# Kernel optimization log

Measured on AMD Instinct MI355X. Metric: run time of the kernel, lower is better.

The kernel has to match this reference:

```python
import jax, jax.numpy as jnp
import numpy as np

LN_EPS = 1e-5

def _ln(x):
    # haiku LayerNorm([-1], create_scale=False, create_offset=False)
    mu = x.mean(axis=-1, keepdims=True)
    var = x.var(axis=-1, keepdims=True)
    return (x - mu) * jax.lax.rsqrt(var + LN_EPS)

def setup_inputs() -> dict:
    key = jax.random.key(0)
    ks = jax.random.split(key, 10)
    N, L, P = 512, 256, 64
    inp = {
        "local": jax.random.normal(ks[0], (N, L), jnp.float32),
        "pair": jax.random.normal(ks[1], (N, N, P), jnp.float32),
        "mask": jax.random.randint(ks[2], (N,), 0, 2, jnp.int32),
        "W_pair_gate": jax.random.normal(ks[3], (P, 2 * P), jnp.float32) / np.sqrt(P),
        "W_pair_value": jax.random.normal(ks[4], (P, 2 * P), jnp.float32) / np.sqrt(P),
        "W_left_gate": jax.random.normal(ks[5], (L, 2 * P), jnp.float32) / np.sqrt(L),
        "W_left_value": jax.random.normal(ks[6], (L, 2 * P), jnp.float32) / np.sqrt(L),
        "W_right_gate": jax.random.normal(ks[7], (L, 2 * P), jnp.float32) / np.sqrt(L),
        "W_right_value": jax.random.normal(ks[8], (L, 2 * P), jnp.float32) / np.sqrt(L),
        "W_out": jax.random.normal(ks[9], (3 * P, P), jnp.float32) / np.sqrt(3 * P),
    }
    return inp

def reference(local, pair, mask, W_pair_gate, W_pair_value, W_left_gate,
              W_left_value, W_right_gate, W_right_value, W_out):
    maskb = mask.astype(bool)
    pair_mask = maskb[:, None] & maskb[None, :]                  # (N, N)
    l = _ln(local)                                               # (N, L)
    p = _ln(pair)                                                # (N, N, P)
    pair_gate = p @ W_pair_gate                                  # (N, N, 2P)
    pair_value = p @ W_pair_value                                # (N, N, 2P)
    # left: broadcast local over axis 0/1, gelu-gate, mask, reduce over j
    left_gate = jax.nn.gelu((l @ W_left_gate)[:, None] + pair_gate)
    left_value = (l @ W_left_value)[None, :] + pair_value
    left = jnp.where(pair_mask[..., None], left_gate * left_value, 0).sum(axis=1)  # (N, 2P)
    right_gate = jax.nn.gelu((l @ W_right_gate)[None, :] + pair_gate)
    right_value = (l @ W_right_value)[:, None] + pair_value
    right = jnp.where(pair_mask[..., None], right_gate * right_value, 0).sum(axis=0)  # (N, 2P)
    paired_pseudo_local = _ln(left[:, None] + right[None, :])    # (N, N, 2P)
    pair_hidden = jnp.concatenate((p, paired_pseudo_local), axis=-1)  # (N, N, 3P)
    return pair_hidden @ W_out                                   # (N, N, P)
```

## Files before the change

### kernel.cpp

```cpp
#include <hip/hip_runtime.h>
#include <math.h>

#define LN_EPS 1e-5f


typedef __bf16 bf16x8 __attribute__((ext_vector_type(8)));
typedef float f32x16 __attribute__((ext_vector_type(16)));

__device__ __forceinline__ float gelu_f(float x) {
    float x2 = x * x;
    float e = __builtin_amdgcn_exp2f(x * fmaf(0.10294423f, x2, 2.3022079f));
    float r = __builtin_amdgcn_rcpf(e + 1.0f);
    return fmaf(-x, r, x);
}

__global__ __launch_bounds__(256) void kA(
    const float* __restrict__ loc,
    const float* __restrict__ Wlg, const float* __restrict__ Wlv,
    const float* __restrict__ Wrg, const float* __restrict__ Wrv,
    float* __restrict__ proj, const int* __restrict__ mask,
    int* __restrict__ act, float* __restrict__ left, float* __restrict__ right) {
    const int t = threadIdx.x;
    if (blockIdx.x == 64) {
        if (blockIdx.y == 1) {
            float4 z = {0.f, 0.f, 0.f, 0.f};
            for (int idx = t; idx < 16384; idx += 256) ((float4*)left)[idx] = z;
        } else if (blockIdx.y == 2) {
            float4 z = {0.f, 0.f, 0.f, 0.f};
            for (int idx = t; idx < 16384; idx += 256) ((float4*)right)[idx] = z;
        } else if (blockIdx.y == 0) {
            __shared__ int cnt_sh[8];
            const int lane = t & 63, wv = t >> 6;
            int msave[2];
            unsigned long long bsave[2];
#pragma unroll
            for (int ch = 0; ch < 2; ++ch) {
                int m = (mask[ch * 256 + t] != 0);
                unsigned long long b = __ballot(m);
                if (lane == 0) cnt_sh[ch * 4 + wv] = __popcll(b);
                msave[ch] = m;
                bsave[ch] = b;
            }
            __syncthreads();
#pragma unroll
            for (int ch = 0; ch < 2; ++ch) {
                int base = 0;
                for (int u = 0; u < ch * 4 + wv; ++u) base += cnt_sh[u];
                int pos = base + __popcll(bsave[ch] & ((1ull << lane) - 1ull));
                if (msave[ch]) act[1 + pos] = ch * 256 + t;
            }
            if (t == 0) {
                int ctot = 0;
                for (int u = 0; u < 8; ++u) ctot += cnt_sh[u];
                act[0] = ctot;
            }
        }
        return;
    }
    __shared__ float ln_sh[8][260];
    __shared__ float red_sh[128][9];
    const int i0 = blockIdx.x * 8;
    const int mat = blockIdx.y;
    const float* __restrict__ W = (mat == 0) ? Wlg : (mat == 1) ? Wlv
                                 : (mat == 2) ? Wrg : Wrv;
    {
        int row = t >> 5, l32 = t & 31;
        const float4* src = (const float4*)(loc + (i0 + row) * 256);
        float4 v0 = src[l32 * 2];
        float4 v1 = src[l32 * 2 + 1];
        float s = (v0.x + v0.y) + (v0.z + v0.w) + (v1.x + v1.y) + (v1.z + v1.w);
        float ss = v0.x * v0.x + v0.y * v0.y + v0.z * v0.z + v0.w * v0.w +
                   v1.x * v1.x + v1.y * v1.y + v1.z * v1.z + v1.w * v1.w;
#pragma unroll
        for (int off = 1; off < 32; off <<= 1) {
            s += __shfl_xor(s, off);
            ss += __shfl_xor(ss, off);
        }
        float mu = s * (1.f / 256.f);
        float rs = rsqrtf(ss * (1.f / 256.f) - mu * mu + LN_EPS);
        float4 o0, o1;
        o0.x = (v0.x - mu) * rs; o0.y = (v0.y - mu) * rs;
        o0.z = (v0.z - mu) * rs; o0.w = (v0.w - mu) * rs;
        o1.x = (v1.x - mu) * rs; o1.y = (v1.y - mu) * rs;
        o1.z = (v1.z - mu) * rs; o1.w = (v1.w - mu) * rs;
        *(float4*)&ln_sh[row][l32 * 8] = o0;
        *(float4*)&ln_sh[row][l32 * 8 + 4] = o1;
    }
    __syncthreads();

    const int n = t & 127;
    const int kh = t >> 7;
    float acc[8] = {0.f, 0.f, 0.f, 0.f, 0.f, 0.f, 0.f, 0.f};
#pragma unroll 2
    for (int c = 0; c < 32; ++c) {
        const int kc = kh * 128 + c * 4;
        float w0 = W[(kc + 0) * 128 + n];
        float w1 = W[(kc + 1) * 128 + n];
        float w2 = W[(kc + 2) * 128 + n];
        float w3 = W[(kc + 3) * 128 + n];
#pragma unroll
        for (int r = 0; r < 8; ++r) {
            float4 l4 = *(const float4*)&ln_sh[r][kc];
            acc[r] += l4.x * w0 + l4.y * w1 + l4.z * w2 + l4.w * w3;
        }
    }
    if (kh == 1) {
#pragma unroll
        for (int r = 0; r < 8; ++r) red_sh[n][r] = acc[r];
    }
    __syncthreads();
    if (kh == 0) {
#pragma unroll
        for (int r = 0; r < 8; ++r)
            proj[mat * 65536 + (i0 + r) * 128 + n] = acc[r] + red_sh[n][r];
    }
}

#define KB_TI 8
__global__ __launch_bounds__(256) void kB(
    const float* __restrict__ pair, const int* __restrict__ act,
    const float* __restrict__ Wg, const float* __restrict__ Wv,
    const float* __restrict__ lg, const float* __restrict__ lv,
    const float* __restrict__ rg, const float* __restrict__ rv,
    float* __restrict__ left, float* __restrict__ right) {
    __shared__ __bf16 A_sh[2][32][72];
    __shared__ int ji_sh[32];
    __shared__ int ii_sh[KB_TI];

    const int cnt = act[0];
    const int j0 = blockIdx.x * 32;
    const int ibase = blockIdx.y * KB_TI;
    if (j0 >= cnt || ibase >= cnt) return;
    const int nact = min(KB_TI, cnt - ibase);

    const int t = threadIdx.x;
    const int lane = t & 63;
    const int w = t >> 6;
    const int c = lane & 31;
    const int half = lane >> 5;
    const int n = w * 32 + c;

    if (t < 32) ji_sh[t] = act[1 + min(j0 + t, cnt - 1)];
    if (t >= 64 && t < 64 + KB_TI) ii_sh[t - 64] = act[1 + min(ibase + (t - 64), cnt - 1)];
    __syncthreads();

    bf16x8 bg[4], bv[4];
#pragma unroll
    for (int kt = 0; kt < 4; ++kt) {
        bf16x8 vg, vv;
#pragma unroll
        for (int e = 0; e < 8; ++e) {
            int kr = kt * 16 + half * 8 + e;
            vg[e] = (__bf16)Wg[kr * 128 + n];
            vv[e] = (__bf16)Wv[kr * 128 + n];
        }
        bg[kt] = vg; bv[kt] = vv;
    }

    float lvr[16], rgr[16];
    unsigned jmask = 0;
#pragma unroll
    for (int r = 0; r < 16; ++r) {
        int m = 4 * half + (r & 3) + 8 * (r >> 2);
        int j = ji_sh[m];
        lvr[r] = lv[j * 128 + n];
        rgr[r] = rg[j * 128 + n];
        if (j0 + m < cnt) jmask |= (1u << r);
    }

    const int srow = t >> 3;
    const int kseg = (t & 7) * 8;
    float4 p0, p1;
    float plg, prv;
    {
        int iF = ii_sh[0];
        const float* src = pair + ((size_t)iF * 512 + ji_sh[srow]) * 64 + kseg;
        p0 = *(const float4*)src;
        p1 = *(const float4*)(src + 4);
        plg = lg[iF * 128 + n];
        prv = rv[iF * 128 + n];
    }

    auto lnwrite = [&](int buf) {
        float s = (p0.x + p0.y) + (p0.z + p0.w) + (p1.x + p1.y) + (p1.z + p1.w);
        float ss = p0.x * p0.x + p0.y * p0.y + p0.z * p0.z + p0.w * p0.w +
                   p1.x * p1.x + p1.y * p1.y + p1.z * p1.z + p1.w * p1.w;
        s += __shfl_xor(s, 1); ss += __shfl_xor(ss, 1);
        s += __shfl_xor(s, 2); ss += __shfl_xor(ss, 2);
        s += __shfl_xor(s, 4); ss += __shfl_xor(ss, 4);
        float mu = s * (1.f / 64.f);
        float rs = rsqrtf(ss * (1.f / 64.f) - mu * mu + LN_EPS);
        bf16x8 o;
        o[0] = (__bf16)((p0.x - mu) * rs); o[1] = (__bf16)((p0.y - mu) * rs);
        o[2] = (__bf16)((p0.z - mu) * rs); o[3] = (__bf16)((p0.w - mu) * rs);
        o[4] = (__bf16)((p1.x - mu) * rs); o[5] = (__bf16)((p1.y - mu) * rs);
        o[6] = (__bf16)((p1.z - mu) * rs); o[7] = (__bf16)((p1.w - mu) * rs);
        *(bf16x8*)&A_sh[buf][srow][kseg] = o;
    };
    lnwrite(0);
    __syncthreads();

    float racc[16];
#pragma unroll
    for (int r = 0; r < 16; ++r) racc[r] = 0.f;

    for (int ii = 0; ii < nact; ++ii) {
        const int i = ii_sh[ii];
        const float lgi = plg;
        const float rvi = prv;
        if (ii + 1 < nact) {
            int iF = ii_sh[ii + 1];
            const float* src = pair + ((size_t)iF * 512 + ji_sh[srow]) * 64 + kseg;
            p0 = *(const float4*)src;
            p1 = *(const float4*)(src + 4);
            plg = lg[iF * 128 + n];
            prv = rv[iF * 128 + n];
        }

        f32x16 ag = {}; f32x16 av = {};
#pragma unroll
        for (int kt = 0; kt < 4; ++kt) {
            bf16x8 af = *(const bf16x8*)&A_sh[ii & 1][c][kt * 16 + half * 8];
            ag = __builtin_amdgcn_mfma_f32_32x32x16_bf16(af, bg[kt], ag, 0, 0, 0);
            av = __builtin_amdgcn_mfma_f32_32x32x16_bf16(af, bv[kt], av, 0, 0, 0);
        }

        float lsum = 0.f;
#pragma unroll
        for (int r = 0; r < 16; ++r) {
            float pg = ag[r], pv = av[r];
            float lres = gelu_f(lgi + pg) * (lvr[r] + pv);
            float rres = gelu_f(rgr[r] + pg) * (rvi + pv);
            lsum += ((jmask >> r) & 1) ? lres : 0.f;
            racc[r] += rres;
        }
        float tot = lsum + __shfl_xor(lsum, 32);
        if (lane < 32) atomicAdd(&left[i * 128 + n], tot);

        if (ii + 1 < nact) lnwrite((ii + 1) & 1);
        __syncthreads();
    }

#pragma unroll
    for (int r = 0; r < 16; ++r) {
        if ((jmask >> r) & 1) {
            int m = 4 * half + (r & 3) + 8 * (r >> 2);
            atomicAdd(&right[ji_sh[m] * 128 + n], racc[r]);
        }
    }
}

__global__ __launch_bounds__(256) void kD(
    const float* __restrict__ left, const float* __restrict__ right,
    const float* __restrict__ W_out,
    float* __restrict__ Aw, float* __restrict__ Bw,
    float* __restrict__ sums, float* __restrict__ cs, float* __restrict__ C) {
    const int bx = blockIdx.x;
    const int t = threadIdx.x;
    if (bx < 256) {
        __shared__ float l_sh[32][68];
        __shared__ float r_sh[32][68];
        const int tx = t & 15, ty = t >> 4;
        const int i0 = (bx & 15) * 32, j0 = (bx >> 4) * 32;
        float acc00 = 0.f, acc01 = 0.f, acc10 = 0.f, acc11 = 0.f;
        for (int kc = 0; kc < 128; kc += 64) {
            __syncthreads();
#pragma unroll
            for (int u = 0; u < 2; ++u) {
                int fi = t + u * 256;
                int row = fi >> 4, kq = (fi & 15) * 4;
                float4 lv4 = *(const float4*)(left + (i0 + row) * 128 + kc + kq);
                float4 rv4 = *(const float4*)(right + (j0 + row) * 128 + kc + kq);
                *(float4*)&l_sh[row][kq] = lv4;
                *(float4*)&r_sh[row][kq] = rv4;
            }
            __syncthreads();
#pragma unroll 8
            for (int k = 0; k < 64; ++k) {
                float l0 = l_sh[ty * 2 + 0][k], l1 = l_sh[ty * 2 + 1][k];
                float r0 = r_sh[tx * 2 + 0][k], r1 = r_sh[tx * 2 + 1][k];
                acc00 += l0 * r0; acc01 += l0 * r1;
                acc10 += l1 * r0; acc11 += l1 * r1;
            }
        }
        C[(size_t)(i0 + ty * 2 + 0) * 512 + j0 + tx * 2 + 0] = acc00;
        C[(size_t)(i0 + ty * 2 + 0) * 512 + j0 + tx * 2 + 1] = acc01;
        C[(size_t)(i0 + ty * 2 + 1) * 512 + j0 + tx * 2 + 0] = acc10;
        C[(size_t)(i0 + ty * 2 + 1) * 512 + j0 + tx * 2 + 1] = acc11;
    } else {
        const int id = bx - 256;
        const int which = id >> 8;
        const int sub = t >> 7;
        const int tt = t & 127;
        const int r = (id & 255) * 2 + sub;
        const float* src = which ? right : left;
        __shared__ float row_sh[2][128];
        __shared__ float red[2][4];
        float v = src[r * 128 + tt];
        row_sh[sub][tt] = v;
        float s = v, ss = v * v;
#pragma unroll
        for (int off = 1; off < 64; off <<= 1) {
            s += __shfl_xor(s, off);
            ss += __shfl_xor(ss, off);
        }
        int wid = tt >> 6, lane = tt & 63;
        if (lane == 0) { red[sub][wid * 2] = s; red[sub][wid * 2 + 1] = ss; }
        __syncthreads();
        if (tt == 0) {
            sums[which * 1024 + r] = red[sub][0] + red[sub][2];
            sums[which * 1024 + 512 + r] = red[sub][1] + red[sub][3];
        }
        if (tt < 64) {
            float a = 0.f;
            const float* W2 = W_out + 64 * 64;
#pragma unroll 8
            for (int m = 0; m < 128; ++m) a += row_sh[sub][m] * W2[m * 64 + tt];
            (which ? Bw : Aw)[r * 64 + tt] = a;
        }
        if (id == 0 && t < 64) {
            float c0 = 0.f, c1 = 0.f;
            for (int k = 0; k < 64; ++k) c0 += W_out[k * 64 + t];
            for (int m = 0; m < 128; ++m) c1 += W_out[(64 + m) * 64 + t];
            cs[t] = c0;
            cs[64 + t] = c1;
        }
    }
}

__global__ __launch_bounds__(256) void kC(
    const float* __restrict__ pair, const float* __restrict__ Wout,
    const float* __restrict__ Aw, const float* __restrict__ Bw,
    const float* __restrict__ Cw, const float* __restrict__ sums,
    const float* __restrict__ cs, float* __restrict__ out) {
    const int t = threadIdx.x;
    const int lane = t & 63;
    const int w = t >> 6;
    const int c = lane & 31;
    const int half = lane >> 5;
    const int i = blockIdx.x;
    const int j0 = blockIdx.y * 64;
    const int mt = w & 1;
    const int nt = w >> 1;
    const int n = nt * 32 + c;
    const int jrow = j0 + mt * 32 + c;

    const float* __restrict__ asrc = pair + ((size_t)i * 512 + jrow) * 64 + half * 8;
    float4 v[8];
#pragma unroll
    for (int kt = 0; kt < 4; ++kt) {
        v[2 * kt] = *(const float4*)(asrc + kt * 16);
        v[2 * kt + 1] = *(const float4*)(asrc + kt * 16 + 4);
    }
    bf16x8 bo[4];
#pragma unroll
    for (int kt = 0; kt < 4; ++kt) {
        bf16x8 bb;
#pragma unroll
        for (int e = 0; e < 8; ++e)
            bb[e] = (__bf16)Wout[(kt * 16 + half * 8 + e) * 64 + n];
        bo[kt] = bb;
    }
    float s = 0.f, ss = 0.f;
#pragma unroll
    for (int u = 0; u < 8; ++u) {
        s += (v[u].x + v[u].y) + (v[u].z + v[u].w);
        ss += v[u].x * v[u].x + v[u].y * v[u].y + v[u].z * v[u].z + v[u].w * v[u].w;
    }
    s += __shfl_xor(s, 32);
    ss += __shfl_xor(ss, 32);
    float mu = s * (1.f / 64.f);
    float rs = rsqrtf(ss * (1.f / 64.f) - mu * mu + LN_EPS);

    f32x16 acc = {};
#pragma unroll
    for (int kt = 0; kt < 4; ++kt) {
        bf16x8 af;
#pragma unroll
        for (int u = 0; u < 2; ++u) {
            float4 vv = v[2 * kt + u];
            af[u * 4 + 0] = (__bf16)((vv.x - mu) * rs);
            af[u * 4 + 1] = (__bf16)((vv.y - mu) * rs);
            af[u * 4 + 2] = (__bf16)((vv.z - mu) * rs);
            af[u * 4 + 3] = (__bf16)((vv.w - mu) * rs);
        }
        acc = __builtin_amdgcn_mfma_f32_32x32x16_bf16(af, bo[kt], acc, 0, 0, 0);
    }

    const float A_in = Aw[i * 64 + n];
    const float cs1n = cs[64 + n];
    const float sumLi = sums[i], ssLi = sums[512 + i];
#pragma unroll
    for (int r = 0; r < 16; ++r) {
        int jp = j0 + mt * 32 + 4 * half + (r & 3) + 8 * (r >> 2);
        float sR = sums[1024 + jp], ssR = sums[1536 + jp];
        float Cv = Cw[(size_t)i * 512 + jp];
        float Bv = Bw[jp * 64 + n];
        float mu_s = (sumLi + sR) * (1.f / 128.f);
        float var_s = fmaf(-mu_s, mu_s, (ssLi + 2.f * Cv + ssR) * (1.f / 128.f));
        float rs_s = rsqrtf(var_s + LN_EPS);
        out[((size_t)i * 512 + jp) * 64 + n] =
            fmaf(rs_s, (A_in + Bv) - mu_s * cs1n, acc[r]);
    }
}

extern "C" void kernel_launch(void* const* d_in, const int* in_sizes, int n_in,
                              void* d_out, int out_size, void* d_ws, size_t ws_size,
                              hipStream_t stream) {
    const float* loc  = (const float*)d_in[0];
    const float* pair = (const float*)d_in[1];
    const int*   mask = (const int*)d_in[2];
    const float* Wpg  = (const float*)d_in[3];
    const float* Wpv  = (const float*)d_in[4];
    const float* Wlg  = (const float*)d_in[5];
    const float* Wlv  = (const float*)d_in[6];
    const float* Wrg  = (const float*)d_in[7];
    const float* Wrv  = (const float*)d_in[8];
    const float* Wout = (const float*)d_in[9];
    float* out = (float*)d_out;
    float* ws = (float*)d_ws;

    float* proj  = ws;
    float* left  = ws + 262144;
    float* right = ws + 327680;
    float* Aw    = ws + 393216;
    float* Bw    = ws + 425984;
    float* Cw    = ws + 458752;
    float* sums  = ws + 720896;
    float* cs    = ws + 722944;
    int*   act   = (int*)(ws + 723072);

    kA<<<dim3(65, 4), 256, 0, stream>>>(loc, Wlg, Wlv, Wrg, Wrv, proj,
                                        mask, act, left, right);
    kB<<<dim3(16, 64), 256, 0, stream>>>(pair, act, Wpg, Wpv,
                                         proj, proj + 65536, proj + 131072,
                                         proj + 196608, left, right);
    kD<<<768, 256, 0, stream>>>(left, right, Wout, Aw, Bw, sums, cs, Cw);
    kC<<<dim3(512, 8), 256, 0, stream>>>(pair, Wout, Aw, Bw, Cw, sums, cs, out);
}
```

Measured before the change: 191.8 us.

## Process four i rows per kC block with double-buffered pair loads

Each kC block now handles four consecutive i rows instead of one, so the grid shrinks fourfold. The Wout bf16 fragments and the Bw values are loaded once and reused across all four rows. While one row's pair data is normalized and multiplied, the next row's data is prefetched into a second register buffer. This cuts redundant weight loads and hides global-load latency, at the cost of higher register pressure and fewer blocks for occupancy.

```diff
diff --git a/kernel.cpp b/kernel.cpp
--- a/kernel.cpp
+++ b/kernel.cpp
@@ -338,20 +338,22 @@
     const int w = t >> 6;
     const int c = lane & 31;
     const int half = lane >> 5;
-    const int i = blockIdx.x;
+    const int i0 = blockIdx.x * 4;
     const int j0 = blockIdx.y * 64;
     const int mt = w & 1;
     const int nt = w >> 1;
     const int n = nt * 32 + c;
     const int jrow = j0 + mt * 32 + c;
 
-    const float* __restrict__ asrc = pair + ((size_t)i * 512 + jrow) * 64 + half * 8;
-    float4 v[8];
+    const float* __restrict__ abase = pair + ((size_t)i0 * 512 + jrow) * 64 + half * 8;
+
+    float4 va[8], vb[8];
 #pragma unroll
     for (int kt = 0; kt < 4; ++kt) {
-        v[2 * kt] = *(const float4*)(asrc + kt * 16);
-        v[2 * kt + 1] = *(const float4*)(asrc + kt * 16 + 4);
-    }
+        va[2 * kt] = *(const float4*)(abase + kt * 16);
+        va[2 * kt + 1] = *(const float4*)(abase + kt * 16 + 4);
+    }
+
     bf16x8 bo[4];
 #pragma unroll
     for (int kt = 0; kt < 4; ++kt) {
@@ -361,47 +363,75 @@
             bb[e] = (__bf16)Wout[(kt * 16 + half * 8 + e) * 64 + n];
         bo[kt] = bb;
     }
-    float s = 0.f, ss = 0.f;
-#pragma unroll
-    for (int u = 0; u < 8; ++u) {
-        s += (v[u].x + v[u].y) + (v[u].z + v[u].w);
-        ss += v[u].x * v[u].x + v[u].y * v[u].y + v[u].z * v[u].z + v[u].w * v[u].w;
-    }
-    s += __shfl_xor(s, 32);
-    ss += __shfl_xor(ss, 32);
-    float mu = s * (1.f / 64.f);
-    float rs = rsqrtf(ss * (1.f / 64.f) - mu * mu + LN_EPS);
-
-    f32x16 acc = {};
-#pragma unroll
-    for (int kt = 0; kt < 4; ++kt) {
-        bf16x8 af;
-#pragma unroll
-        for (int u = 0; u < 2; ++u) {
-            float4 vv = v[2 * kt + u];
-            af[u * 4 + 0] = (__bf16)((vv.x - mu) * rs);
-            af[u * 4 + 1] = (__bf16)((vv.y - mu) * rs);
-            af[u * 4 + 2] = (__bf16)((vv.z - mu) * rs);
-            af[u * 4 + 3] = (__bf16)((vv.w - mu) * rs);
-        }
-        acc = __builtin_amdgcn_mfma_f32_32x32x16_bf16(af, bo[kt], acc, 0, 0, 0);
-    }
-
-    const float A_in = Aw[i * 64 + n];
-    const float cs1n = cs[64 + n];
-    const float sumLi = sums[i], ssLi = sums[512 + i];
+    float Bv[16];
 #pragma unroll
     for (int r = 0; r < 16; ++r) {
         int jp = j0 + mt * 32 + 4 * half + (r & 3) + 8 * (r >> 2);
-        float sR = sums[1024 + jp], ssR = sums[1536 + jp];
-        float Cv = Cw[(size_t)i * 512 + jp];
-        float Bv = Bw[jp * 64 + n];
-        float mu_s = (sumLi + sR) * (1.f / 128.f);
-        float var_s = fmaf(-mu_s, mu_s, (ssLi + 2.f * Cv + ssR) * (1.f / 128.f));
-        float rs_s = rsqrtf(var_s + LN_EPS);
-        out[((size_t)i * 512 + jp) * 64 + n] =
-            fmaf(rs_s, (A_in + Bv) - mu_s * cs1n, acc[r]);
-    }
+        Bv[r] = Bw[jp * 64 + n];
+    }
+    const float cs1n = cs[64 + n];
+
+    auto body = [&](float4 (&cur)[8], float4 (&nxt)[8], int ii) {
+        if (ii < 3) {
+            const float* src = abase + (size_t)(ii + 1) * 512 * 64;
+#pragma unroll
+            for (int kt = 0; kt < 4; ++kt) {
+                nxt[2 * kt] = *(const float4*)(src + kt * 16);
+                nxt[2 * kt + 1] = *(const float4*)(src + kt * 16 + 4);
+            }
+        }
+        const int i = i0 + ii;
+        float Cv[16];
+#pragma unroll
+        for (int r = 0; r < 16; ++r) {
+            int jp = j0 + mt * 32 + 4 * half + (r & 3) + 8 * (r >> 2);
+            Cv[r] = Cw[(size_t)i * 512 + jp];
+        }
+        const float A_in = Aw[i * 64 + n];
+        const float sumLi = sums[i], ssLi = sums[512 + i];
+
+        float s = 0.f, ss = 0.f;
+#pragma unroll
+        for (int u = 0; u < 8; ++u) {
+            s += (cur[u].x + cur[u].y) + (cur[u].z + cur[u].w);
+            ss += cur[u].x * cur[u].x + cur[u].y * cur[u].y +
+                  cur[u].z * cur[u].z + cur[u].w * cur[u].w;
+        }
+        s += __shfl_xor(s, 32);
+        ss += __shfl_xor(ss, 32);
+        float mu = s * (1.f / 64.f);
+        float rs = rsqrtf(ss * (1.f / 64.f) - mu * mu + LN_EPS);
+
+        f32x16 acc = {};
+#pragma unroll
+        for (int kt = 0; kt < 4; ++kt) {
+            bf16x8 af;
+#pragma unroll
+            for (int u = 0; u < 2; ++u) {
+                float4 vv = cur[2 * kt + u];
+                af[u * 4 + 0] = (__bf16)((vv.x - mu) * rs);
+                af[u * 4 + 1] = (__bf16)((vv.y - mu) * rs);
+                af[u * 4 + 2] = (__bf16)((vv.z - mu) * rs);
+                af[u * 4 + 3] = (__bf16)((vv.w - mu) * rs);
+            }
+            acc = __builtin_amdgcn_mfma_f32_32x32x16_bf16(af, bo[kt], acc, 0, 0, 0);
+        }
+
+#pragma unroll
+        for (int r = 0; r < 16; ++r) {
+            int jp = j0 + mt * 32 + 4 * half + (r & 3) + 8 * (r >> 2);
+            float sR = sums[1024 + jp], ssR = sums[1536 + jp];
+            float mu_s = (sumLi + sR) * (1.f / 128.f);
+            float var_s = fmaf(-mu_s, mu_s, (ssLi + 2.f * Cv[r] + ssR) * (1.f / 128.f));
+            float rs_s = rsqrtf(var_s + LN_EPS);
+            out[((size_t)i * 512 + jp) * 64 + n] =
+                fmaf(rs_s, (A_in + Bv[r]) - mu_s * cs1n, acc[r]);
+        }
+    };
+    body(va, vb, 0);
+    body(vb, va, 1);
+    body(va, vb, 2);
+    body(vb, va, 3);
 }
 
 extern "C" void kernel_launch(void* const* d_in, const int* in_sizes, int n_in,
@@ -436,5 +466,5 @@
                                          proj, proj + 65536, proj + 131072,
                                          proj + 196608, left, right);
     kD<<<768, 256, 0, stream>>>(left, right, Wout, Aw, Bw, sums, cs, Cw);
-    kC<<<dim3(512, 8), 256, 0, stream>>>(pair, Wout, Aw, Bw, Cw, sums, cs, out);
-}
+    kC<<<dim3(128, 8), 256, 0, stream>>>(pair, Wout, Aw, Bw, Cw, sums, cs, out);
+}
```

Result: no change. 189.9 us (-1.0%).
